# Kernel optimization log

Hardware: AMD Instinct MI355X
Metric: run time of the kernel (lower is better)

## Reference

```python
import jax, jax.numpy as jnp
import numpy as np

IN_F = 135; D = 512; K = 10; DCT_N = 34; IN_N = 120; OUT_N = 24
VL = K + OUT_N          # 34, window length
VN = IN_N - K - OUT_N + 1  # 87, number of windows
NSTAGE = 2
BN_SCALE = 1.0 / np.sqrt(1.0 + 1e-5)  # eval-mode BN with default running stats (mean 0, var 1)


def get_dct_matrix(N):
    dct_m = np.eye(N)
    for k in range(N):
        for i in range(N):
            w = np.sqrt(2.0 / N)
            if k == 0:
                w = np.sqrt(1.0 / N)
            dct_m[k, i] = w * np.cos(np.pi * (i + 0.5) * k / N)
    idct_m = np.linalg.inv(dct_m)
    return dct_m, idct_m

_DCT_NP, _IDCT_NP = get_dct_matrix(VL)
DCT = jnp.asarray(_DCT_NP[:DCT_N], dtype=jnp.float32)        # [34,34] (dct_n == vl)
IDCT = jnp.asarray(_IDCT_NP[:, :DCT_N], dtype=jnp.float32)   # [34,34]

WIN_IDX = np.arange(VL)[None, :] + np.arange(VN)[:, None]    # [87,34]
PAD_IDX = np.concatenate([np.arange(IN_N - K, IN_N), np.full(OUT_N, IN_N - 1)])  # last 10 frames + last frame repeated


def conv1d(x, w):
    return jax.lax.conv_general_dilated(x, w, (1,), 'VALID',
                                        dimension_numbers=('NCH', 'OIH', 'NCH'))


def gconv(x, att, w, b):
    # GraphConvolution: att @ (x @ w) + b ; x: [b,n,f_in]
    return jnp.einsum('nm,bmf->bnf', att, x @ w) + b


def bn_eval(y, g, b):
    bs, n, f = y.shape
    v = y.reshape(bs, n * f)
    v = g * (v * BN_SCALE) + b
    return v.reshape(bs, n, f)


def setup_inputs() -> dict:
    key = jax.random.key(0)
    ks = jax.random.split(key, 20)
    s = 0.05  # small init scale so tanh/att stay in sane range
    return {
        'poses':    jax.random.normal(ks[0], (256, 144, 135), jnp.float32),
        'qw1':      jax.random.normal(ks[1], (512, 135, 6)) * s,
        'qw2':      jax.random.normal(ks[2], (512, 512, 5)) * s,
        'kw1':      jax.random.normal(ks[3], (512, 135, 6)) * s,
        'kw2':      jax.random.normal(ks[4], (512, 512, 5)) * s,
        'gc1_att':  jax.random.normal(ks[5], (135, 135)) * s,
        'gc1_w':    jax.random.normal(ks[6], (68, 512)) * s,
        'gc1_b':    jax.random.normal(ks[7], (512,)) * s,
        'bn1_g':    jnp.ones((69120,), jnp.float32),
        'bn1_b':    jnp.zeros((69120,), jnp.float32),
        'gcb_att':  jax.random.normal(ks[8], (4, 135, 135)) * s,
        'gcb_w':    jax.random.normal(ks[9], (4, 512, 512)) * s,
        'gcb_b':    jax.random.normal(ks[10], (4, 512)) * s,
        'gcb_g':    jnp.ones((4, 69120), jnp.float32),
        'gcb_beta': jnp.zeros((4, 69120), jnp.float32),
        'gc7_att':  jax.random.normal(ks[11], (135, 135)) * s,
        'gc7_w':    jax.random.normal(ks[12], (512, 68)) * s,
        'gc7_b':    jax.random.normal(ks[13], (68,)) * s,
    }


def reference(poses, qw1, qw2, kw1, kw2,
              gc1_att, gc1_w, gc1_b, bn1_g, bn1_b,
              gcb_att, gcb_w, gcb_b, gcb_g, gcb_beta,
              gc7_att, gc7_w, gc7_b):
    src = poses[:, :IN_N]                      # [b,120,135]
    bs = src.shape[0]
    src_t = jnp.transpose(src, (0, 2, 1))      # [b,135,120]
    key_in = src_t[:, :, :IN_N - OUT_N] / 1000.0   # [b,135,96]
    qry_in = src_t[:, :, -K:] / 1000.0             # [b,135,10]

    key_f = jax.nn.relu(conv1d(jax.nn.relu(conv1d(key_in, kw1)), kw2))  # [b,512,87]
    qry_f = jax.nn.relu(conv1d(jax.nn.relu(conv1d(qry_in, qw1)), qw2))  # [b,512,1]

    # non-softmax attention: matmul + eps-normalize
    score = jnp.einsum('bdq,bdk->bqk', qry_f, key_f) + 1e-15   # [b,1,87]
    att = score / jnp.sum(score, axis=2, keepdims=True)

    # overlapping windows -> DCT of each window
    windows = src[:, WIN_IDX]                                   # [b,87,34,135]
    val = jnp.einsum('kt,bvtf->bvfk', DCT, windows).reshape(bs, VN, IN_F * DCT_N)
    dct_att = jnp.einsum('bqv,bvz->bqz', att, val)[:, 0].reshape(bs, IN_F, DCT_N)

    input_gcn = src[:, PAD_IDX]                                 # [b,34,135]
    dct_in = jnp.einsum('kt,btf->bfk', DCT, input_gcn)          # [b,135,34]
    x = jnp.concatenate([dct_in, dct_att], axis=-1)             # [b,135,68]

    # GCN (eval mode: dropout = identity, BN uses running stats)
    y = jnp.tanh(bn_eval(gconv(x, gc1_att, gc1_w, gc1_b), bn1_g, bn1_b))
    for i in range(NSTAGE):
        res = y
        h = jnp.tanh(bn_eval(gconv(y, gcb_att[2 * i], gcb_w[2 * i], gcb_b[2 * i]),
                             gcb_g[2 * i], gcb_beta[2 * i]))
        h = jnp.tanh(bn_eval(gconv(h, gcb_att[2 * i + 1], gcb_w[2 * i + 1], gcb_b[2 * i + 1]),
                             gcb_g[2 * i + 1], gcb_beta[2 * i + 1]))
        y = h + res
    y = gconv(y, gc7_att, gc7_w, gc7_b) + x                     # [b,135,68]

    out = jnp.einsum('tk,bfk->btf', IDCT, y[:, :, :DCT_N])      # [b,34,135]
    preds = out[:, -OUT_N:, :]                                  # [b,24,135]
    return preds
```

## Files before the change

### kernel.cpp

```cpp
#include <hip/hip_runtime.h>
#include <math.h>

#define POSE_ROWS 144
#define NF 135
#define DD 512
#define KQ 10
#define DCTN 34
#define INN 120
#define OUTN 24
#define VN 87
#define BATCH 256
#define RP 34816
#define NODEP 136
#define BN_SCALE 0.9999950000374997f

typedef __attribute__((ext_vector_type(8))) short short8;
typedef __attribute__((ext_vector_type(4))) float floatx4;

static __device__ __forceinline__ ushort f2bf(float f) {
    unsigned u = __builtin_bit_cast(unsigned, f);
    u = (u + 0x7FFFu + ((u >> 16) & 1u)) >> 16;
    return (ushort)u;
}
static __device__ __forceinline__ float bf2f(ushort s) {
    return __builtin_bit_cast(float, (unsigned)s << 16);
}
static __device__ __forceinline__ float tanh_fast(float x) {
    float ax = __builtin_fabsf(x);
    float e = __builtin_amdgcn_exp2f(ax * -2.885390081777927f);
    float t = (1.f - e) * __builtin_amdgcn_rcpf(1.f + e);
    return __builtin_copysignf(t, x);
}

#define GLOAD_LDS(gp, lp) __builtin_amdgcn_global_load_lds( \
    (const __attribute__((address_space(1))) unsigned int*)(const void*)(gp), \
    (__attribute__((address_space(3))) unsigned int*)(void*)(lp), 16, 0, 0)

#define PB_POSES 19584
#define PB_K1B   22912
#define PB_K2B   33152
#define PB_WT1   33408
#define PB_WTB   37504
#define PB_WT7   37640
#define PB_A1    37742
#define PB_AB    38147
#define PB_A7    38249
#define PB_BN    39609
#define PB_Z     39610
#define PB_DCT   39615

__global__ __launch_bounds__(256) void prep_all(
    const float* __restrict__ poses, ushort* __restrict__ pb16,
    const float* __restrict__ kw1, const float* __restrict__ qw1,
    ushort* __restrict__ Wt1k, ushort* __restrict__ Wt1q,
    const float* __restrict__ kw2, const float* __restrict__ qw2,
    ushort* __restrict__ Wt2k, ushort* __restrict__ Wt2q,
    const float* __restrict__ gc1_w, ushort* __restrict__ WT1,
    const float* __restrict__ gcb_w, ushort* __restrict__ WTb,
    const float* __restrict__ gc7_w, ushort* __restrict__ WT7,
    const float* __restrict__ gc1_att, ushort* __restrict__ A16_1,
    const float* __restrict__ gcb_att, ushort* __restrict__ A16_B,
    const float* __restrict__ gc7_att, ushort* __restrict__ A16_7,
    const float* __restrict__ bn1_g, const float* __restrict__ bn1_b,
    const float* __restrict__ gcb_g, const float* __restrict__ gcb_beta,
    float* __restrict__ bnT, float* __restrict__ zpadf, float* __restrict__ dct)
{
    const int blk = blockIdx.x;
    const int tid = threadIdx.x;
    if (blk < PB_POSES) {
        int idx = blk * 256 + tid;
        int i = idx % NODEP;
        int row = (idx / NODEP) % POSE_ROWS;
        int b = idx / (NODEP * POSE_ROWS);
        float v = (i < NF) ? poses[((long long)b * POSE_ROWS + row) * NF + i] * 1e-3f : 0.f;
        pb16[idx] = f2bf(v);
    } else if (blk < PB_K1B) {
        int wi = blk - PB_POSES;
        const float* src = (wi < 1664) ? kw1 : qw1;
        ushort* dst = (wi < 1664) ? Wt1k : Wt1q;
        int idx = (wi % 1664) * 256 + tid;
        int n = idx / 832, k = idx % 832;
        int h = k / 136, i = k % 136;
        float v = (i < 135 && h < 6) ? src[((long long)n * 135 + i) * 6 + h] : 0.f;
        dst[idx] = f2bf(v);
    } else if (blk < PB_K2B) {
        int wi = blk - PB_K1B;
        const float* src = (wi < 5120) ? kw2 : qw2;
        ushort* dst = (wi < 5120) ? Wt2k : Wt2q;
        int idx = (wi % 5120) * 256 + tid;
        int n = idx / 2560, k = idx % 2560;
        int h = k / 512, i = k % 512;
        dst[idx] = f2bf(src[((long long)n * 512 + i) * 5 + h]);
    } else if (blk < PB_WT1) {
        int idx = (blk - PB_K2B) * 256 + tid;
        int n = idx / 128, k = idx % 128;
        WT1[idx] = f2bf((k < 68) ? gc1_w[(long long)k * 512 + n] : 0.f);
    } else if (blk < PB_WTB) {
        int g = (blk - PB_WT1) * 256 + tid;
        int L = g >> 18, idx = g & 262143;
        int n = idx / 512, k = idx % 512;
        WTb[g] = f2bf(gcb_w[(long long)L * 262144 + (long long)k * 512 + n]);
    } else if (blk < PB_WT7) {
        int idx = (blk - PB_WTB) * 256 + tid;
        int n = idx / 512, k = idx % 512;
        WT7[idx] = f2bf(gc7_w[(long long)k * 68 + n]);
    } else if (blk < PB_A1) {
        int idx = (blk - PB_WT7) * 256 + tid;
        if (idx < 135 * 192) {
            int r = idx / 192, c = idx % 192;
            A16_1[idx] = f2bf(c < 135 ? gc1_att[r * 135 + c] : 0.f);
        }
    } else if (blk < PB_AB) {
        int idx = (blk - PB_A1) * 256 + tid;
        int r = idx / 192, c = idx % 192;
        A16_B[idx] = f2bf(c < 135 ? gcb_att[r * 135 + c] : 0.f);
    } else if (blk < PB_A7) {
        int idx = (blk - PB_AB) * 256 + tid;
        if (idx < 135 * 192) {
            int r = idx / 192, c = idx % 192;
            A16_7[idx] = f2bf(c < 135 ? gc7_att[r * 135 + c] : 0.f);
        }
    } else if (blk < PB_BN) {
        int g = (blk - PB_A7) * 256 + tid;
        int p = g / 69632, idx = g % 69632;
        int node = idx % 136, m = idx / 136;
        const float* gs = (p == 0) ? bn1_g : (gcb_g + (p - 1) * 69120);
        const float* bs = (p == 0) ? bn1_b : (gcb_beta + (p - 1) * 69120);
        float* gt = bnT + (long long)p * 139264;
        float* bt = gt + 69632;
        gt[idx] = (node < 135) ? gs[node * 512 + m] : 0.f;
        bt[idx] = (node < 135) ? bs[node * 512 + m] : 0.f;
    } else if (blk < PB_Z) {
        if (tid < 128) zpadf[tid] = 0.f;
    } else {
        int idx = (blk - PB_Z) * 256 + tid;
        if (idx < DCTN * DCTN) {
            int k = idx / DCTN, i = idx % DCTN;
            double w = (k == 0) ? sqrt(1.0 / DCTN) : sqrt(2.0 / DCTN);
            dct[idx] = (float)(w * cos(3.14159265358979323846 * (i + 0.5) * k / (double)DCTN));
        }
    }
}

template<int BM, int BN>
__global__ __launch_bounds__(256) void gemm2(
    const ushort* __restrict__ A, const ushort* __restrict__ Bt,
    const ushort* __restrict__ zpad,
    int M, int N, int K,
    int mode, int CNT, int Pc,
    int rpbA, long long sAw, long long sAr, long long sAbz,
    long long sBr, long long sBbz,
    float* __restrict__ C, ushort* __restrict__ C16,
    long long sCbz, long long sCm, long long sCn,
    int do_relu, const float* __restrict__ bias, int bias_mode,
    const float* __restrict__ bnTg, const float* __restrict__ bnTb,
    int do_tanh, const ushort* __restrict__ resid16, const float* __restrict__ resid32)
{
    constexpr int SM = BM / 32, SN = BN / 32;
    constexpr int RA = BM / 32, RB = BN / 32;
    __shared__ ushort As[BM * 64];
    __shared__ ushort Bs[BN * 64];

    int mb, nb;
    if (mode == 0) { mb = blockIdx.y; nb = blockIdx.x; }
    else {
        int gx = blockIdx.x;
        int x = gx & 7, s = gx >> 3;
        if (mode == 1) { mb = s % CNT; nb = x * Pc + s / CNT; }
        else           { nb = s % CNT; mb = x * Pc + s / CNT; }
    }
    const int m0 = mb * BM, n0 = nb * BN;
    if (m0 >= M || n0 >= N) return;

    const int tid = threadIdx.x;
    const int lane = tid & 63, w = tid >> 6;
    const int bz = blockIdx.z;
    const int wm = (w >> 1) * (BM / 2), wn = (w & 1) * (BN / 2);
    const int chunk = (lane & 7) ^ ((lane >> 3) & 7);

    const ushort* pA[RA]; int stA[RA];
    #pragma unroll
    for (int j = 0; j < RA; j++) {
        int m = m0 + j * 32 + w * 8 + (lane >> 3);
        bool v = m < M;
        long long off = v ? ((long long)(m / rpbA) * sAw + (long long)(m % rpbA) * sAr
                            + (long long)bz * sAbz) : 0;
        pA[j] = v ? (A + off + chunk * 8) : (zpad + chunk * 8);
        stA[j] = v ? 64 : 0;
    }
    const ushort* pB[RB]; int stB[RB];
    #pragma unroll
    for (int j = 0; j < RB; j++) {
        int n = n0 + j * 32 + w * 8 + (lane >> 3);
        bool v = n < N;
        long long off = v ? ((long long)n * sBr + (long long)bz * sBbz) : 0;
        pB[j] = v ? (Bt + off + chunk * 8) : (zpad + chunk * 8);
        stB[j] = v ? 64 : 0;
    }

    floatx4 acc[SM][SN];
    #pragma unroll
    for (int i = 0; i < SM; i++)
        #pragma unroll
        for (int j = 0; j < SN; j++)
            acc[i][j] = (floatx4){0.f, 0.f, 0.f, 0.f};

    for (int k0 = 0; k0 < K; k0 += 64) {
        #pragma unroll
        for (int j = 0; j < RA; j++)
            GLOAD_LDS(pA[j], &As[(j * 32 + w * 8) * 64]);
        #pragma unroll
        for (int j = 0; j < RB; j++)
            GLOAD_LDS(pB[j], &Bs[(j * 32 + w * 8) * 64]);
        __syncthreads();

        #pragma unroll
        for (int kk = 0; kk < 2; kk++) {
            short8 af[SM], bf[SN];
            #pragma unroll
            for (int sm = 0; sm < SM; sm++) {
                int lr = wm + sm * 16 + (lane & 15);
                int slot = ((lane >> 4) + kk * 4) ^ (lr & 7);
                af[sm] = *(const short8*)&As[lr * 64 + slot * 8];
            }
            #pragma unroll
            for (int sn = 0; sn < SN; sn++) {
                int lr = wn + sn * 16 + (lane & 15);
                int slot = ((lane >> 4) + kk * 4) ^ (lr & 7);
                bf[sn] = *(const short8*)&Bs[lr * 64 + slot * 8];
            }
            #pragma unroll
            for (int sm = 0; sm < SM; sm++)
                #pragma unroll
                for (int sn = 0; sn < SN; sn++)
                    acc[sm][sn] = __builtin_amdgcn_mfma_f32_16x16x32_bf16(af[sm], bf[sn], acc[sm][sn], 0, 0, 0);
        }
        __syncthreads();

        #pragma unroll
        for (int j = 0; j < RA; j++) pA[j] += stA[j];
        #pragma unroll
        for (int j = 0; j < RB; j++) pB[j] += stB[j];
    }

    const int lc = lane & 15;
    const int lr4 = (lane >> 4) << 2;
    #pragma unroll
    for (int sm = 0; sm < SM; sm++) {
        #pragma unroll
        for (int sn = 0; sn < SN; sn++) {
            int n = n0 + wn + sn * 16 + lc;
            if (n >= N) continue;
            int node = n % 136;
            int mbv = m0 + wm + sm * 16 + lr4;
            float vv[4];
            #pragma unroll
            for (int r = 0; r < 4; r++) {
                int m = mbv + r;
                float v = acc[sm][sn][r];
                if (do_relu) v = fmaxf(v, 0.f);
                if (bias) v += (bias_mode == 1) ? bias[m < M ? m : 0] : bias[n];
                if (bnTg) {
                    long long gi = (long long)(m < M ? m : 0) * 136 + node;
                    v = bnTg[gi] * (v * BN_SCALE) + bnTb[gi];
                }
                if (do_tanh) v = tanh_fast(v);
                long long addr = (long long)bz * sCbz + (long long)m * sCm + (long long)n * sCn;
                if (m < M) {
                    if (resid16) v += bf2f(resid16[addr]);
                    else if (resid32) v += resid32[addr];
                    if (C) C[addr] = v;
                    if (C16 && sCm != 1) C16[addr] = f2bf(v);
                }
                vv[r] = v;
            }
            if (C16 && sCm == 1 && mbv + 3 < M) {
                ushort4 pk;
                pk.x = f2bf(vv[0]); pk.y = f2bf(vv[1]); pk.z = f2bf(vv[2]); pk.w = f2bf(vv[3]);
                *(ushort4*)&C16[(long long)bz * sCbz + mbv + (long long)n * sCn] = pk;
            }
        }
    }
}

__global__ __launch_bounds__(256) void att_k(const float* __restrict__ kf, const float* __restrict__ qf,
                                             float* __restrict__ att) {
    int b = blockIdx.x;
    int tid = threadIdx.x;
    int lane = tid & 63, w = tid >> 6;
    __shared__ float s[96];
    __shared__ float ssum;
    const float* qb = qf + b * DD + lane * 8;
    float4 q0 = *(const float4*)qb;
    float4 q1 = *(const float4*)(qb + 4);
    const float* kb = kf + (long long)b * VN * DD;
    for (int v = w; v < VN; v += 4) {
        const float* kr = kb + v * DD + lane * 8;
        float4 k0 = *(const float4*)kr;
        float4 k1 = *(const float4*)(kr + 4);
        float p = q0.x * k0.x + q0.y * k0.y + q0.z * k0.z + q0.w * k0.w
                + q1.x * k1.x + q1.y * k1.y + q1.z * k1.z + q1.w * k1.w;
        #pragma unroll
        for (int off = 32; off; off >>= 1) p += __shfl_xor(p, off);
        if (lane == 0) s[v] = p + 1e-15f;
    }
    __syncthreads();
    if (tid < 64) {
        float p2 = (tid < VN ? s[tid] : 0.f) + ((tid + 64) < VN ? s[tid + 64] : 0.f);
        #pragma unroll
        for (int off = 32; off; off >>= 1) p2 += __shfl_xor(p2, off);
        if (tid == 0) ssum = p2;
    }
    __syncthreads();
    float inv = 1.f / ssum;
    for (int v = tid; v < VN; v += 256) att[b * VN + v] = s[v] * inv;
}

__global__ void weighted_k(const float* __restrict__ poses, const float* __restrict__ att,
                           float* __restrict__ w34) {
    int t = blockIdx.x;
    int b = blockIdx.y;
    int f = threadIdx.x;
    if (f >= NF) return;
    const float* pb = poses + (long long)b * POSE_ROWS * NF + t * NF + f;
    const float* ab = att + b * VN;
    float acc = 0.f;
    for (int v = 0; v < VN; v++) acc += ab[v] * pb[v * NF];
    w34[(long long)b * DCTN * NF + t * NF + f] = acc;
}

__global__ void build_x(const float* __restrict__ poses, const float* __restrict__ w34,
                        const float* __restrict__ dctm, float* __restrict__ x32,
                        ushort* __restrict__ xT16) {
    int idx = blockIdx.x * 256 + threadIdx.x;
    if (idx >= BATCH * NF * 68) return;
    int kk = idx % 68;
    int f = (idx / 68) % NF;
    int b = idx / (68 * NF);
    float acc = 0.f;
    if (kk < DCTN) {
        const float* pb = poses + (long long)b * POSE_ROWS * NF;
        #pragma unroll
        for (int t = 0; t < DCTN; t++) {
            int row = (t < KQ) ? (INN - KQ + t) : (INN - 1);
            acc += dctm[kk * DCTN + t] * pb[row * NF + f];
        }
    } else {
        int k2 = kk - DCTN;
        const float* wb = w34 + (long long)b * DCTN * NF + f;
        #pragma unroll
        for (int t = 0; t < DCTN; t++) acc += dctm[k2 * DCTN + t] * wb[t * NF];
    }
    long long R = (long long)b * NODEP + f;
    x32[R * 68 + kk] = acc;
    xT16[(long long)kk * RP + R] = f2bf(acc);
}

__global__ void idct_out(const float* __restrict__ h32, const float* __restrict__ dctm,
                         float* __restrict__ out) {
    int idx = blockIdx.x * 256 + threadIdx.x;
    if (idx >= BATCH * OUTN * NF) return;
    int f = idx % NF;
    int t = (idx / NF) % OUTN;
    int b = idx / (NF * OUTN);
    const float* yr = h32 + ((long long)b * NODEP + f) * 68;
    float acc = 0.f;
    #pragma unroll
    for (int k = 0; k < DCTN; k++) acc += dctm[k * DCTN + (KQ + t)] * yr[k];
    out[idx] = acc;
}

extern "C" void kernel_launch(void* const* d_in, const int* in_sizes, int n_in,
                              void* d_out, int out_size, void* d_ws, size_t ws_size,
                              hipStream_t stream) {
    const float* poses   = (const float*)d_in[0];
    const float* qw1     = (const float*)d_in[1];
    const float* qw2     = (const float*)d_in[2];
    const float* kw1     = (const float*)d_in[3];
    const float* kw2     = (const float*)d_in[4];
    const float* gc1_att = (const float*)d_in[5];
    const float* gc1_w   = (const float*)d_in[6];
    const float* gc1_b   = (const float*)d_in[7];
    const float* bn1_g   = (const float*)d_in[8];
    const float* bn1_b   = (const float*)d_in[9];
    const float* gcb_att = (const float*)d_in[10];
    const float* gcb_w   = (const float*)d_in[11];
    const float* gcb_b   = (const float*)d_in[12];
    const float* gcb_g   = (const float*)d_in[13];
    const float* gcb_beta= (const float*)d_in[14];
    const float* gc7_att = (const float*)d_in[15];
    const float* gc7_w   = (const float*)d_in[16];
    const float* gc7_b   = (const float*)d_in[17];
    float* out = (float*)d_out;
    float* w = (float*)d_ws;

    float* dct   = w;
    float* att   = w + 1280;
    float* w34   = w + 23808;
    float* x32   = w + 1198848;
    float* h32   = w + 3566336;
    float* qf    = w + 5933824;
    ushort* su   = (ushort*)(w + 6064896);
    ushort* WT1    = su;
    ushort* WTb    = su + 65536;
    ushort* WT7    = su + 1114112;
    ushort* A16_1  = su + 1148928;
    ushort* A16_B  = su + 1174848;
    ushort* A16_7  = su + 1278528;
    float* bnT   = w + 6717120;
    float* kf    = w + 7413440;
    ushort* R2   = (ushort*)(w + 18816704);
    ushort* yT16  = R2;
    ushort* r1k16 = R2;
    ushort* r1q16 = R2 + 11927552;
    ushort* R3   = (ushort*)(w + 27729600);
    ushort* hT16  = R3;
    ushort* pb16  = R3;
    ushort* Wt1k  = R3 + 5013504;
    ushort* Wt1q  = R3 + 5439488;
    ushort* Wt2k  = R3 + 5865472;
    ushort* Wt2q  = R3 + 7176192;
    ushort* R4   = (ushort*)(w + 36642496);
    ushort* zN16  = R4;
    ushort* xT16  = R4;
    ushort* z116  = R4 + 2367488;
    float* zpadf = w + 45555392;
    const ushort* zpad = (const ushort*)zpadf;

    const int INF_RPB = 1 << 30;

    prep_all<<<PB_DCT, 256, 0, stream>>>(
        poses, pb16, kw1, qw1, Wt1k, Wt1q, kw2, qw2, Wt2k, Wt2q,
        gc1_w, WT1, gcb_w, WTb, gc7_w, WT7,
        gc1_att, A16_1, gcb_att, A16_B, gc7_att, A16_7,
        bn1_g, bn1_b, gcb_g, gcb_beta, bnT, zpadf, dct);

    gemm2<128,64><<<dim3(1472, 1, 1), 256, 0, stream>>>(pb16, Wt1k, zpad, 23296, 512, 832,
        2, 8, 23, 91, 19584LL, 136LL, 0LL, 832LL, 0LL,
        (float*)nullptr, r1k16, 0LL, 512LL, 1LL, 1, nullptr, 0, nullptr, nullptr, 0, nullptr, nullptr);
    gemm2<128,128><<<dim3(4, 10, 1), 256, 0, stream>>>(pb16 + 110*136, Wt1q, zpad, 1280, 512, 832,
        0, 0, 0, 5, 19584LL, 136LL, 0LL, 832LL, 0LL,
        (float*)nullptr, r1q16, 0LL, 512LL, 1LL, 1, nullptr, 0, nullptr, nullptr, 0, nullptr, nullptr);
    gemm2<128,64><<<dim3(1408, 1, 1), 256, 0, stream>>>(r1k16, Wt2k, zpad, 22272, 512, 2560,
        2, 8, 22, 87, 46592LL, 512LL, 0LL, 2560LL, 0LL,
        kf, (ushort*)nullptr, 0LL, 512LL, 1LL, 1, nullptr, 0, nullptr, nullptr, 0, nullptr, nullptr);
    gemm2<64,64><<<dim3(8, 4, 1), 256, 0, stream>>>(r1q16, Wt2q, zpad, 256, 512, 2560,
        0, 0, 0, INF_RPB, 0LL, 2560LL, 0LL, 2560LL, 0LL,
        qf, (ushort*)nullptr, 0LL, 512LL, 1LL, 1, nullptr, 0, nullptr, nullptr, 0, nullptr, nullptr);

    att_k<<<BATCH, 256, 0, stream>>>(kf, qf, att);
    weighted_k<<<dim3(DCTN, BATCH), 192, 0, stream>>>(poses, att, w34);
    build_x<<<(BATCH * NF * 68 + 255) / 256, 256, 0, stream>>>(poses, w34, dct, x32, xT16);

    gemm2<64,64><<<dim3(3, 2, BATCH), 256, 0, stream>>>(xT16, A16_1, zpad, 68, 135, 192,
        0, 0, 0, INF_RPB, 0LL, (long long)RP, 136LL, 192LL, 0LL,
        (float*)nullptr, z116, 10880LL, 1LL, 80LL, 0, nullptr, 0, nullptr, nullptr, 0, nullptr, nullptr);
    gemm2<128,64><<<dim3(2176, 1, 1), 256, 0, stream>>>(WT1, z116, zpad, 512, RP, 128,
        1, 4, 68, INF_RPB, 0LL, 128LL, 0LL, 80LL, 0LL,
        (float*)nullptr, yT16, 0LL, (long long)RP, 1LL, 0, gc1_b, 1, bnT, bnT + 69632, 1, nullptr, nullptr);

    for (int L = 0; L < 4; L++) {
        const ushort* min = (L & 1) ? hT16 : yT16;
        gemm2<64,64><<<dim3(3, 8, BATCH), 256, 0, stream>>>(min, A16_B + L*25920, zpad, 512, 135, 192,
            0, 0, 0, INF_RPB, 0LL, (long long)RP, 136LL, 192LL, 0LL,
            (float*)nullptr, zN16, 69632LL, 1LL, 512LL, 0, nullptr, 0, nullptr, nullptr, 0, nullptr, nullptr);
        gemm2<128,64><<<dim3(2176, 1, 1), 256, 0, stream>>>(WTb + L*262144, zN16, zpad, 512, RP, 512,
            1, 4, 68, INF_RPB, 0LL, 512LL, 0LL, 512LL, 0LL,
            (float*)nullptr, (L & 1) ? yT16 : hT16, 0LL, (long long)RP, 1LL,
            0, gcb_b + L*512, 1, bnT + (1 + L) * 139264, bnT + (1 + L) * 139264 + 69632, 1,
            (L & 1) ? yT16 : (const ushort*)nullptr, nullptr);
    }

    gemm2<64,64><<<dim3(3, 8, BATCH), 256, 0, stream>>>(yT16, A16_7, zpad, 512, 135, 192,
        0, 0, 0, INF_RPB, 0LL, (long long)RP, 136LL, 192LL, 0LL,
        (float*)nullptr, zN16, 69632LL, 1LL, 512LL, 0, nullptr, 0, nullptr, nullptr, 0, nullptr, nullptr);
    gemm2<64,64><<<dim3(1088, 1, 1), 256, 0, stream>>>(zN16, WT7, zpad, RP, 68, 512,
        2, 2, 68, INF_RPB, 0LL, 512LL, 0LL, 512LL, 0LL,
        h32, (ushort*)nullptr, 0LL, 68LL, 1LL, 0, gc7_b, 2, nullptr, nullptr, 0, nullptr, x32);

    idct_out<<<(BATCH * OUTN * NF + 255) / 256, 256, 0, stream>>>(h32, dct, out);
}
```

Baseline: 1.023 ms.

## Add K-resident 64x64 GEMM kernel for GCN layers with split-K-half prefetch

```diff
diff --git a/kernel.cpp b/kernel.cpp
--- a/kernel.cpp
+++ b/kernel.cpp
@@ -283,6 +283,150 @@
     }
 }
 
+template<int KK, int NH>
+__global__ __launch_bounds__(256) void gemm_res(
+    const ushort* __restrict__ A, const ushort* __restrict__ Bt,
+    const ushort* __restrict__ zpad,
+    int M, int N,
+    int mode, int CNT, int Pc,
+    long long sAr, long long sAbz,
+    long long sBr, long long sBbz,
+    float* __restrict__ C, ushort* __restrict__ C16,
+    long long sCbz, long long sCm, long long sCn,
+    int do_relu, const float* __restrict__ bias, int bias_mode,
+    const float* __restrict__ bnTg, const float* __restrict__ bnTb,
+    int do_tanh, const ushort* __restrict__ resid16, const float* __restrict__ resid32)
+{
+    constexpr int HC = KK / (8 * NH);
+    constexpr int ROUNDS = 64 * HC / 256;
+    constexpr int TSTEP = KK / 64 / NH;
+    __shared__ ushort As[NH][64 * HC * 8];
+    __shared__ ushort Bs[NH][64 * HC * 8];
+
+    int mb, nb;
+    if (mode == 0) { mb = blockIdx.y; nb = blockIdx.x; }
+    else {
+        int gx = blockIdx.x;
+        int x = gx & 7, s = gx >> 3;
+        if (mode == 1) { mb = s % CNT; nb = x * Pc + s / CNT; }
+        else           { nb = s % CNT; mb = x * Pc + s / CNT; }
+    }
+    const int m0 = mb * 64, n0 = nb * 64;
+    if (m0 >= M || n0 >= N) return;
+
+    const int tid = threadIdx.x;
+    const int lane = tid & 63, w = tid >> 6;
+    const int bz = blockIdx.z;
+    const int wm = (w >> 1) * 32, wn = (w & 1) * 32;
+
+    #pragma unroll
+    for (int h = 0; h < NH; h++) {
+        #pragma unroll
+        for (int r = 0; r < ROUNDS; r++) {
+            int u = r * 256 + w * 64 + lane;
+            int row = u / HC, cin = u % HC;
+            int m = m0 + row;
+            const ushort* src = (m < M)
+                ? (A + (long long)m * sAr + (long long)bz * sAbz
+                     + (h * HC + (cin ^ (row & 7))) * 8)
+                : zpad;
+            GLOAD_LDS(src, &As[h][(r * 256 + w * 64) * 8]);
+        }
+        #pragma unroll
+        for (int r = 0; r < ROUNDS; r++) {
+            int u = r * 256 + w * 64 + lane;
+            int row = u / HC, cin = u % HC;
+            int n = n0 + row;
+            const ushort* src = (n < N)
+                ? (Bt + (long long)n * sBr + (long long)bz * sBbz
+                      + (h * HC + (cin ^ (row & 7))) * 8)
+                : zpad;
+            GLOAD_LDS(src, &Bs[h][(r * 256 + w * 64) * 8]);
+        }
+        __builtin_amdgcn_sched_barrier(0);
+    }
+
+    floatx4 acc[2][2];
+    #pragma unroll
+    for (int i = 0; i < 2; i++)
+        #pragma unroll
+        for (int j = 0; j < 2; j++)
+            acc[i][j] = (floatx4){0.f, 0.f, 0.f, 0.f};
+
+    #pragma unroll
+    for (int h = 0; h < NH; h++) {
+        if (h == 0) {
+            asm volatile("s_waitcnt vmcnt(%0)" :: "n"(2 * ROUNDS * (NH - 1)) : "memory");
+        } else {
+            asm volatile("s_waitcnt vmcnt(0)" ::: "memory");
+        }
+        __builtin_amdgcn_sched_barrier(0);
+        __builtin_amdgcn_s_barrier();
+        #pragma unroll
+        for (int t = 0; t < TSTEP; t++) {
+            #pragma unroll
+            for (int kk = 0; kk < 2; kk++) {
+                int c4 = t * 8 + kk * 4 + (lane >> 4);
+                short8 af[2], bf[2];
+                #pragma unroll
+                for (int sm = 0; sm < 2; sm++) {
+                    int lr = wm + sm * 16 + (lane & 15);
+                    af[sm] = *(const short8*)&As[h][(lr * HC + (c4 ^ (lr & 7))) * 8];
+                }
+                #pragma unroll
+                for (int sn = 0; sn < 2; sn++) {
+                    int lr = wn + sn * 16 + (lane & 15);
+                    bf[sn] = *(const short8*)&Bs[h][(lr * HC + (c4 ^ (lr & 7))) * 8];
+                }
+                #pragma unroll
+                for (int sm = 0; sm < 2; sm++)
+                    #pragma unroll
+                    for (int sn = 0; sn < 2; sn++)
+                        acc[sm][sn] = __builtin_amdgcn_mfma_f32_16x16x32_bf16(af[sm], bf[sn], acc[sm][sn], 0, 0, 0);
+            }
+        }
+    }
+
+    const int lc = lane & 15;
+    const int lr4 = (lane >> 4) << 2;
+    #pragma unroll
+    for (int sm = 0; sm < 2; sm++) {
+        #pragma unroll
+        for (int sn = 0; sn < 2; sn++) {
+            int n = n0 + wn + sn * 16 + lc;
+            if (n >= N) continue;
+            int node = n % 136;
+            int mbv = m0 + wm + sm * 16 + lr4;
+            float vv[4];
+            #pragma unroll
+            for (int r = 0; r < 4; r++) {
+                int m = mbv + r;
+                float v = acc[sm][sn][r];
+                if (do_relu) v = fmaxf(v, 0.f);
+                if (bias) v += (bias_mode == 1) ? bias[m < M ? m : 0] : bias[n];
+                if (bnTg) {
+                    long long gi = (long long)(m < M ? m : 0) * 136 + node;
+                    v = bnTg[gi] * (v * BN_SCALE) + bnTb[gi];
+                }
+                if (do_tanh) v = tanh_fast(v);
+                long long addr = (long long)bz * sCbz + (long long)m * sCm + (long long)n * sCn;
+                if (m < M) {
+                    if (resid16) v += bf2f(resid16[addr]);
+                    else if (resid32) v += resid32[addr];
+                    if (C) C[addr] = v;
+                    if (C16 && sCm != 1) C16[addr] = f2bf(v);
+                }
+                vv[r] = v;
+            }
+            if (C16 && sCm == 1 && mbv + 3 < M) {
+                ushort4 pk;
+                pk.x = f2bf(vv[0]); pk.y = f2bf(vv[1]); pk.z = f2bf(vv[2]); pk.w = f2bf(vv[3]);
+                *(ushort4*)&C16[(long long)bz * sCbz + mbv + (long long)n * sCn] = pk;
+            }
+        }
+    }
+}
+
 __global__ __launch_bounds__(256) void att_k(const float* __restrict__ kf, const float* __restrict__ qf,
                                              float* __restrict__ att) {
     int b = blockIdx.x;
@@ -452,30 +596,30 @@
     weighted_k<<<dim3(DCTN, BATCH), 192, 0, stream>>>(poses, att, w34);
     build_x<<<(BATCH * NF * 68 + 255) / 256, 256, 0, stream>>>(poses, w34, dct, x32, xT16);
 
-    gemm2<64,64><<<dim3(3, 2, BATCH), 256, 0, stream>>>(xT16, A16_1, zpad, 68, 135, 192,
-        0, 0, 0, INF_RPB, 0LL, (long long)RP, 136LL, 192LL, 0LL,
+    gemm_res<192,1><<<dim3(3, 2, BATCH), 256, 0, stream>>>(xT16, A16_1, zpad, 68, 135,
+        0, 0, 0, (long long)RP, 136LL, 192LL, 0LL,
         (float*)nullptr, z116, 10880LL, 1LL, 80LL, 0, nullptr, 0, nullptr, nullptr, 0, nullptr, nullptr);
-    gemm2<128,64><<<dim3(2176, 1, 1), 256, 0, stream>>>(WT1, z116, zpad, 512, RP, 128,
-        1, 4, 68, INF_RPB, 0LL, 128LL, 0LL, 80LL, 0LL,
+    gemm_res<128,1><<<dim3(4352, 1, 1), 256, 0, stream>>>(WT1, z116, zpad, 512, RP,
+        1, 8, 68, 128LL, 0LL, 80LL, 0LL,
         (float*)nullptr, yT16, 0LL, (long long)RP, 1LL, 0, gc1_b, 1, bnT, bnT + 69632, 1, nullptr, nullptr);
 
     for (int L = 0; L < 4; L++) {
         const ushort* min = (L & 1) ? hT16 : yT16;
-        gemm2<64,64><<<dim3(3, 8, BATCH), 256, 0, stream>>>(min, A16_B + L*25920, zpad, 512, 135, 192,
-            0, 0, 0, INF_RPB, 0LL, (long long)RP, 136LL, 192LL, 0LL,
+        gemm_res<192,1><<<dim3(3, 8, BATCH), 256, 0, stream>>>(min, A16_B + L*25920, zpad, 512, 135,
+            0, 0, 0, (long long)RP, 136LL, 192LL, 0LL,
             (float*)nullptr, zN16, 69632LL, 1LL, 512LL, 0, nullptr, 0, nullptr, nullptr, 0, nullptr, nullptr);
-        gemm2<128,64><<<dim3(2176, 1, 1), 256, 0, stream>>>(WTb + L*262144, zN16, zpad, 512, RP, 512,
-            1, 4, 68, INF_RPB, 0LL, 512LL, 0LL, 512LL, 0LL,
+        gemm_res<512,2><<<dim3(4352, 1, 1), 256, 0, stream>>>(WTb + L*262144, zN16, zpad, 512, RP,
+            1, 8, 68, 512LL, 0LL, 512LL, 0LL,
             (float*)nullptr, (L & 1) ? yT16 : hT16, 0LL, (long long)RP, 1LL,
             0, gcb_b + L*512, 1, bnT + (1 + L) * 139264, bnT + (1 + L) * 139264 + 69632, 1,
             (L & 1) ? yT16 : (const ushort*)nullptr, nullptr);
     }
 
-    gemm2<64,64><<<dim3(3, 8, BATCH), 256, 0, stream>>>(yT16, A16_7, zpad, 512, 135, 192,
-        0, 0, 0, INF_RPB, 0LL, (long long)RP, 136LL, 192LL, 0LL,
+    gemm_res<192,1><<<dim3(3, 8, BATCH), 256, 0, stream>>>(yT16, A16_7, zpad, 512, 135,
+        0, 0, 0, (long long)RP, 136LL, 192LL, 0LL,
         (float*)nullptr, zN16, 69632LL, 1LL, 512LL, 0, nullptr, 0, nullptr, nullptr, 0, nullptr, nullptr);
-    gemm2<64,64><<<dim3(1088, 1, 1), 256, 0, stream>>>(zN16, WT7, zpad, RP, 68, 512,
-        2, 2, 68, INF_RPB, 0LL, 512LL, 0LL, 512LL, 0LL,
+    gemm_res<512,2><<<dim3(1088, 1, 1), 256, 0, stream>>>(zN16, WT7, zpad, RP, 68,
+        2, 2, 68, 512LL, 0LL, 512LL, 0LL,
         h32, (ushort*)nullptr, 0LL, 68LL, 1LL, 0, gc7_b, 2, nullptr, nullptr, 0, nullptr, x32);
 
     idct_out<<<(BATCH * OUTN * NF + 255) / 256, 256, 0, stream>>>(h32, dct, out);
```

Result: slower. 1.496 ms (+46.3%).

## Fuse per-sample graph attention and weight GEMMs into one LDS-resident layer kernel

Applied to the files above, without the earlier changes.

```diff
diff --git a/kernel.cpp b/kernel.cpp
--- a/kernel.cpp
+++ b/kernel.cpp
@@ -283,6 +283,153 @@
     }
 }
 
+__global__ __launch_bounds__(512, 2) void fused_layer(
+    const ushort* __restrict__ Yin,
+    const ushort* __restrict__ Att,
+    const ushort* __restrict__ Wt,
+    const ushort* __restrict__ zpad,
+    const float* __restrict__ bias,
+    const float* __restrict__ bnTg, const float* __restrict__ bnTb,
+    const ushort* __restrict__ resid16,
+    ushort* __restrict__ Yout)
+{
+    extern __shared__ ushort zs[];
+    const int b = blockIdx.x;
+    const int tid = threadIdx.x;
+    const int lane = tid & 63, w = tid >> 6;
+    const int ln = lane & 15;
+    const int lk8 = (lane >> 4) * 8;
+    const int lr4 = (lane >> 4) << 2;
+    const long long ybase = (long long)b * 136;
+
+    {
+        const int cp = w * 64;
+        const ushort* pb[9];
+        #pragma unroll
+        for (int nt = 0; nt < 9; nt++) {
+            int n = nt * 16 + ln;
+            pb[nt] = (n < 135) ? (Att + (long long)n * 192 + lk8) : (zpad + lk8);
+        }
+        const ushort* pa[4];
+        #pragma unroll
+        for (int sm = 0; sm < 4; sm++) {
+            int c = cp + sm * 16 + ln;
+            pa[sm] = Yin + (long long)c * RP + ybase + lk8;
+        }
+        floatx4 acc[4][9];
+        #pragma unroll
+        for (int i = 0; i < 4; i++)
+            #pragma unroll
+            for (int j = 0; j < 9; j++)
+                acc[i][j] = (floatx4){0.f, 0.f, 0.f, 0.f};
+
+        #pragma unroll
+        for (int kc = 0; kc < 3; kc++) {
+            #pragma unroll
+            for (int kk = 0; kk < 2; kk++) {
+                if (kc == 2 && kk == 1) continue;
+                const int ko = kc * 64 + kk * 32;
+                short8 af[4], bf[9];
+                #pragma unroll
+                for (int sm = 0; sm < 4; sm++)
+                    af[sm] = *(const short8*)(pa[sm] + ko);
+                #pragma unroll
+                for (int nt = 0; nt < 9; nt++)
+                    bf[nt] = *(const short8*)(pb[nt] + ko);
+                #pragma unroll
+                for (int sm = 0; sm < 4; sm++)
+                    #pragma unroll
+                    for (int nt = 0; nt < 9; nt++)
+                        acc[sm][nt] = __builtin_amdgcn_mfma_f32_16x16x32_bf16(af[sm], bf[nt], acc[sm][nt], 0, 0, 0);
+            }
+        }
+        #pragma unroll
+        for (int sm = 0; sm < 4; sm++) {
+            #pragma unroll
+            for (int nt = 0; nt < 9; nt++) {
+                int n = nt * 16 + ln;
+                if (n >= 136) continue;
+                int c = cp + sm * 16 + lr4;
+                ushort4 pk;
+                pk.x = f2bf(acc[sm][nt][0]);
+                pk.y = f2bf(acc[sm][nt][1]);
+                pk.z = f2bf(acc[sm][nt][2]);
+                pk.w = f2bf(acc[sm][nt][3]);
+                int chs = (c >> 3) ^ (n & 7);
+                *(ushort4*)&zs[n * 512 + chs * 8 + (c & 7)] = pk;
+            }
+        }
+    }
+    __syncthreads();
+
+    {
+        const int p = (w >> 1) * 128;
+        const int nt0 = (w & 1) ? 4 : 0;
+        const ushort* pw[8];
+        #pragma unroll
+        for (int sm = 0; sm < 8; sm++)
+            pw[sm] = Wt + (long long)(p + sm * 16 + ln) * 512 + lk8;
+        int zrow[5], zx[5];
+        #pragma unroll
+        for (int j = 0; j < 5; j++) {
+            int n = (nt0 + j) * 16 + ln;
+            int nn = (n < 136) ? n : 0;
+            zrow[j] = nn * 512;
+            zx[j] = nn & 7;
+        }
+        floatx4 acc[8][5];
+        #pragma unroll
+        for (int i = 0; i < 8; i++)
+            #pragma unroll
+            for (int j = 0; j < 5; j++)
+                acc[i][j] = (floatx4){0.f, 0.f, 0.f, 0.f};
+
+        #pragma unroll
+        for (int kc = 0; kc < 8; kc++) {
+            #pragma unroll
+            for (int kk = 0; kk < 2; kk++) {
+                const int ko = kc * 64 + kk * 32;
+                const int kchunk = kc * 8 + kk * 4 + (lane >> 4);
+                short8 af[8], bf[5];
+                #pragma unroll
+                for (int sm = 0; sm < 8; sm++)
+                    af[sm] = *(const short8*)(pw[sm] + ko);
+                #pragma unroll
+                for (int j = 0; j < 5; j++)
+                    bf[j] = *(const short8*)&zs[zrow[j] + (kchunk ^ zx[j]) * 8];
+                #pragma unroll
+                for (int sm = 0; sm < 8; sm++)
+                    #pragma unroll
+                    for (int j = 0; j < 5; j++)
+                        acc[sm][j] = __builtin_amdgcn_mfma_f32_16x16x32_bf16(af[sm], bf[j], acc[sm][j], 0, 0, 0);
+            }
+        }
+        #pragma unroll
+        for (int sm = 0; sm < 8; sm++) {
+            #pragma unroll
+            for (int j = 0; j < 5; j++) {
+                int nt = nt0 + j;
+                if (nt == 4 && (w & 1) == 0) continue;
+                int n = nt * 16 + ln;
+                if (n >= 136) continue;
+                int c2 = p + sm * 16 + lr4;
+                #pragma unroll
+                for (int r = 0; r < 4; r++) {
+                    int m = c2 + r;
+                    float v = acc[sm][j][r];
+                    v += bias[m];
+                    long long gi = (long long)m * 136 + n;
+                    v = bnTg[gi] * (v * BN_SCALE) + bnTb[gi];
+                    v = tanh_fast(v);
+                    long long addr = (long long)m * RP + ybase + n;
+                    if (resid16) v += bf2f(resid16[addr]);
+                    Yout[addr] = f2bf(v);
+                }
+            }
+        }
+    }
+}
+
 __global__ __launch_bounds__(256) void att_k(const float* __restrict__ kf, const float* __restrict__ qf,
                                              float* __restrict__ att) {
     int b = blockIdx.x;
@@ -429,6 +576,13 @@
 
     const int INF_RPB = 1 << 30;
 
+    static int lds_set = 0;
+    if (!lds_set) {
+        hipFuncSetAttribute((const void*)fused_layer,
+                            hipFuncAttributeMaxDynamicSharedMemorySize, 139264);
+        lds_set = 1;
+    }
+
     prep_all<<<PB_DCT, 256, 0, stream>>>(
         poses, pb16, kw1, qw1, Wt1k, Wt1q, kw2, qw2, Wt2k, Wt2q,
         gc1_w, WT1, gcb_w, WTb, gc7_w, WT7,
@@ -461,14 +615,11 @@
 
     for (int L = 0; L < 4; L++) {
         const ushort* min = (L & 1) ? hT16 : yT16;
-        gemm2<64,64><<<dim3(3, 8, BATCH), 256, 0, stream>>>(min, A16_B + L*25920, zpad, 512, 135, 192,
-            0, 0, 0, INF_RPB, 0LL, (long long)RP, 136LL, 192LL, 0LL,
-            (float*)nullptr, zN16, 69632LL, 1LL, 512LL, 0, nullptr, 0, nullptr, nullptr, 0, nullptr, nullptr);
-        gemm2<128,64><<<dim3(2176, 1, 1), 256, 0, stream>>>(WTb + L*262144, zN16, zpad, 512, RP, 512,
-            1, 4, 68, INF_RPB, 0LL, 512LL, 0LL, 512LL, 0LL,
-            (float*)nullptr, (L & 1) ? yT16 : hT16, 0LL, (long long)RP, 1LL,
-            0, gcb_b + L*512, 1, bnT + (1 + L) * 139264, bnT + (1 + L) * 139264 + 69632, 1,
-            (L & 1) ? yT16 : (const ushort*)nullptr, nullptr);
+        ushort* mout = (L & 1) ? yT16 : hT16;
+        fused_layer<<<dim3(BATCH, 1, 1), 512, 139264, stream>>>(
+            min, A16_B + L * 25920, WTb + L * 262144, zpad,
+            gcb_b + L * 512, bnT + (1 + L) * 139264, bnT + (1 + L) * 139264 + 69632,
+            (L & 1) ? yT16 : (const ushort*)nullptr, mout);
     }
 
     gemm2<64,64><<<dim3(3, 8, BATCH), 256, 0, stream>>>(yT16, A16_7, zpad, 512, 135, 192,
```

Measured after the change: 1.019 ms. Within noise of the previous version (-0.4%).
